# Kernel optimization log

Measured on AMD Instinct MI355X. Metric: run time of the kernel, lower is better.

Reference implementation:

```python
import jax, jax.numpy as jnp
import numpy as np
from jax import lax

B = 2048
C = 8
H = W = 14
NP = H * W  # 196
DIM = 192
THETA = 0.7


def _unfold3(z):
    # z: [B, C, H, W] -> patches [B, C, 9, H, W], matching F.unfold(kernel=3, pad=1)
    p = jnp.pad(z, ((0, 0), (0, 0), (1, 1), (1, 1)))
    return jnp.stack([p[:, :, dy:dy + H, dx:dx + W]
                      for dy in range(3) for dx in range(3)], axis=2)


def setup_inputs() -> dict:
    key = jax.random.key(0)
    ks = jax.random.split(key, 10)
    s = 0.1
    return {
        "x": jax.random.normal(ks[0], (B, 1 + NP, DIM), dtype=jnp.float32),
        "W1": jax.random.normal(ks[1], (C, DIM), dtype=jnp.float32) * s,      # linear1 192->8
        "b1": jax.random.normal(ks[2], (C,), dtype=jnp.float32) * s,
        "conv1_w": jax.random.normal(ks[3], (C, C), dtype=jnp.float32) * s,   # 1x1 conv
        "conv1_b": jax.random.normal(ks[4], (C,), dtype=jnp.float32) * s,
        "cdc_w": jax.random.normal(ks[5], (C, C, 1, 5), dtype=jnp.float32) * s,
        "wc1": jax.random.normal(ks[6], (C, C), dtype=jnp.float32) * s,       # WConv1 (1x1)
        "wc2": jax.random.normal(ks[7], (C, C), dtype=jnp.float32) * s,       # WConv2 (1x1)
        "hist_w": jax.random.normal(ks[8], (DIM, C), dtype=jnp.float32) * s,  # linear 8->192
        "hist_b": jax.random.normal(ks[9], (DIM,), dtype=jnp.float32) * s,
    }


def reference(x, W1, b1, conv1_w, conv1_b, cdc_w, wc1, wc2, hist_w, hist_b):
    class_token, tok = x[:, :1, :], x[:, 1:, :]
    # linear1: [B,196,192] -> [B,196,8]
    t = jnp.einsum('bnd,cd->bnc', tok, W1) + b1
    # -> [B,8,14,14]
    t = t.reshape(-1, H, W, C).transpose(0, 3, 1, 2)

    # conv1 (1x1)
    x1 = jnp.einsum('bihw,oi->bohw', t, conv1_w) + conv1_b[None, :, None, None]

    # CDC: scatter the 1x5 weights into a 3x3 cross-shaped kernel
    w5 = cdc_w[:, :, 0, :]  # [O,I,5]
    z = jnp.zeros((C, C, 1), dtype=cdc_w.dtype)
    k9 = jnp.concatenate([z, w5[:, :, 0:1], z,
                          w5[:, :, 1:2], w5[:, :, 2:3], w5[:, :, 3:4],
                          z, w5[:, :, 4:5], z], axis=2).reshape(C, C, 3, 3)
    out_normal = lax.conv_general_dilated(
        t, k9, window_strides=(1, 1), padding=((1, 1), (1, 1)),
        dimension_numbers=('NCHW', 'OIHW', 'NCHW'))
    kernel_diff = cdc_w.sum(axis=(2, 3))  # [O,I]
    out_diff = jnp.einsum('bihw,oi->bohw', t, kernel_diff)
    x2 = out_normal - THETA * out_diff

    z_star = x1 + x2  # [B,8,14,14]

    # TokenHistogram
    mu = jnp.einsum('bihw,oi->bohw', z_star, wc1)
    gamma = jnp.einsum('bihw,oi->bohw', z_star, wc2)
    zp = _unfold3(z_star)   # [B,8,9,14,14]
    mp = _unfold3(mu)
    gp = _unfold3(gamma)
    u = gp * (zp - mp)
    z_hist = jnp.exp(-u * u).sum(axis=2) / 9.0  # [B,8,14,14]
    # torch .reshape(-1, NP, 8): plain row-major reshape (mixes C and HW)
    z_hist = z_hist.reshape(-1, NP, C)
    y = jnp.einsum('bnc,dc->bnd', z_hist, hist_w) + hist_b  # [B,196,192]

    return jnp.concatenate([class_token, y], axis=1)
```

## Files before the change

kernel.cpp:

```cpp
#include <hip/hip_runtime.h>


#define DIMD 192
#define IMGS 37824

__launch_bounds__(256)
__global__ void k1_head(
    const float* __restrict__ x,
    const float* __restrict__ W1,
    const float* __restrict__ b1,
    const float* __restrict__ conv1_w,
    const float* __restrict__ conv1_b,
    const float* __restrict__ cdc_w,
    const float* __restrict__ wc1,
    const float* __restrict__ wc2,
    float* __restrict__ zh_ws,
    float* __restrict__ out)
{
    __shared__ float smem[4608];
    float* TS  = smem;
    float* PS  = smem + 2048;
    float* WB2 = smem + 4096;

    const int tid = threadIdx.x;
    const float* xb   = x   + (size_t)blockIdx.x * IMGS;
    float*       outb = out + (size_t)blockIdx.x * IMGS;

    {
        float4 z4 = make_float4(0.f, 0.f, 0.f, 0.f);
        float4 o4 = make_float4(1.f, 1.f, 1.f, 1.f);
        ((float4*)TS)[tid]       = z4;
        ((float4*)TS)[tid + 256] = z4;
        ((float4*)PS)[tid]       = o4;
        ((float4*)PS)[tid + 256] = o4;
    }
    if (tid < 64) {
        const float* c5 = cdc_w + tid * 5;
        float k0 = c5[0], k1 = c5[1], k2 = c5[2], k3 = c5[3], k4 = c5[4];
        float kd = k0 + k1 + k2 + k3 + k4;
        float* wp = WB2 + tid * 8;
        wp[0] = conv1_w[tid] + k2 - 0.7f * kd;
        wp[1] = k0; wp[2] = k1; wp[3] = k3; wp[4] = k4;
        wp[5] = wc1[tid];
        wp[6] = wc2[tid];
        wp[7] = 0.f;
    }
    __syncthreads();

    if (tid < 196) {
        const float4* rowp = (const float4*)(xb + DIMD + tid * DIMD);
        float acc[8];
        #pragma unroll
        for (int c = 0; c < 8; ++c) acc[c] = b1[c];
        #pragma unroll
        for (int blk = 0; blk < 6; ++blk) {
            float4 tv[8];
            #pragma unroll
            for (int u = 0; u < 8; ++u) tv[u] = rowp[blk * 8 + u];
            #pragma unroll
            for (int c = 0; c < 8; ++c) {
                const float* wrow = W1 + c * DIMD + blk * 32;
                #pragma unroll
                for (int u = 0; u < 8; ++u) {
                    acc[c] += tv[u].x * wrow[u * 4 + 0] + tv[u].y * wrow[u * 4 + 1]
                            + tv[u].z * wrow[u * 4 + 2] + tv[u].w * wrow[u * 4 + 3];
                }
            }
        }
        int h = tid / 14, w = tid - h * 14;
        float* tp = TS + (h + 1) * 16 + (w + 1);
        #pragma unroll
        for (int c = 0; c < 8; ++c) tp[c * 256] = acc[c];
    } else if (tid >= 208) {
        ((float4*)outb)[tid - 208] = ((const float4*)xb)[tid - 208];
    }
    __syncthreads();

    if (tid < 196) {
        int h = tid / 14, w = tid - h * 14;
        const float* tp = TS + (h + 1) * 16 + (w + 1);
        float zv[8];
        #pragma unroll
        for (int c = 0; c < 8; ++c) zv[c] = conv1_b[c];
        #pragma unroll
        for (int i = 0; i < 8; ++i) {
            float t0 = tp[i * 256];
            float tu = tp[i * 256 - 16];
            float td = tp[i * 256 + 16];
            float tl = tp[i * 256 - 1];
            float tr = tp[i * 256 + 1];
            #pragma unroll
            for (int c = 0; c < 8; ++c) {
                const float* wp = WB2 + (c * 8 + i) * 8;
                float4 wv = *(const float4*)wp;
                float wd = wp[4];
                zv[c] += wv.x * t0 + wv.y * tu + wv.z * tl + wv.w * tr + wd * td;
            }
        }
        float* pp = PS + (h + 1) * 16 + (w + 1);
        #pragma unroll
        for (int c = 0; c < 8; ++c) {
            float mu = 0.f, ga = 0.f;
            #pragma unroll
            for (int i = 0; i < 8; ++i) {
                const float* wp = WB2 + (c * 8 + i) * 8;
                mu += wp[5] * zv[i];
                ga += wp[6] * zv[i];
            }
            float e = ga * (zv[c] - mu);
            pp[c * 256] = __expf(-e * e);
        }
    }
    __syncthreads();

    if (tid < 196) {
        int h = tid / 14, w = tid - h * 14;
        const float* pb = PS + h * 16 + w;
        float* zg = zh_ws + (size_t)blockIdx.x * 1568;
        #pragma unroll
        for (int c = 0; c < 8; ++c) {
            const float* pr = pb + c * 256;
            float s9 = pr[0]  + pr[1]  + pr[2]
                     + pr[16] + pr[17] + pr[18]
                     + pr[32] + pr[33] + pr[34];
            zg[c * 196 + tid] = s9 * (1.f / 9.f);
        }
    }
}

__launch_bounds__(192)
__global__ void k2_hist(
    const float* __restrict__ zh_ws,
    const float* __restrict__ hist_w,
    const float* __restrict__ hist_b,
    float* __restrict__ out)
{
    __shared__ float zsh[1568];
    const int d = threadIdx.x;
    const float* zg = zh_ws + (size_t)blockIdx.x * 1568;

    for (int f = d; f < 392; f += 192)
        ((float4*)zsh)[f] = ((const float4*)zg)[f];

    const float4 h0 = *(const float4*)(hist_w + d * 8);
    const float4 h1 = *(const float4*)(hist_w + d * 8 + 4);
    const float  hb = hist_b[d];
    __syncthreads();

    float* oy = out + (size_t)blockIdx.x * IMGS + DIMD;
    #pragma unroll 4
    for (int n2 = 0; n2 < 196; ++n2) {
        const float4 z0 = *(const float4*)(zsh + n2 * 8);
        const float4 z1 = *(const float4*)(zsh + n2 * 8 + 4);
        oy[n2 * DIMD + d] = hb
            + z0.x * h0.x + z0.y * h0.y + z0.z * h0.z + z0.w * h0.w
            + z1.x * h1.x + z1.y * h1.y + z1.z * h1.z + z1.w * h1.w;
    }
}

__launch_bounds__(256)
__global__ void sadapter_fused(
    const float* __restrict__ x,
    const float* __restrict__ W1,
    const float* __restrict__ b1,
    const float* __restrict__ conv1_w,
    const float* __restrict__ conv1_b,
    const float* __restrict__ cdc_w,
    const float* __restrict__ wc1,
    const float* __restrict__ wc2,
    const float* __restrict__ hist_w,
    const float* __restrict__ hist_b,
    float* __restrict__ out)
{
    __shared__ float smem[4608];
    float* TS  = smem;
    float* ZH  = smem;
    float* PS  = smem + 2048;
    float* WB2 = smem + 4096;
    const int tid = threadIdx.x;
    const float* xb   = x   + (size_t)blockIdx.x * IMGS;
    float*       outb = out + (size_t)blockIdx.x * IMGS;

    {
        float4 z4 = make_float4(0.f,0.f,0.f,0.f), o4 = make_float4(1.f,1.f,1.f,1.f);
        ((float4*)TS)[tid] = z4; ((float4*)TS)[tid+256] = z4;
        ((float4*)PS)[tid] = o4; ((float4*)PS)[tid+256] = o4;
    }
    if (tid < 64) {
        const float* c5 = cdc_w + tid * 5;
        float k0=c5[0],k1=c5[1],k2=c5[2],k3=c5[3],k4=c5[4];
        float kd = k0+k1+k2+k3+k4;
        float* wp = WB2 + tid*8;
        wp[0]=conv1_w[tid]+k2-0.7f*kd; wp[1]=k0; wp[2]=k1; wp[3]=k3; wp[4]=k4;
        wp[5]=wc1[tid]; wp[6]=wc2[tid]; wp[7]=0.f;
    }
    __syncthreads();
    if (tid < 196) {
        const float4* rowp = (const float4*)(xb + DIMD + tid * DIMD);
        float acc[8];
        #pragma unroll
        for (int c=0;c<8;++c) acc[c]=b1[c];
        #pragma unroll
        for (int blk=0; blk<6; ++blk) {
            float4 tv[8];
            #pragma unroll
            for (int u=0;u<8;++u) tv[u]=rowp[blk*8+u];
            #pragma unroll
            for (int c=0;c<8;++c) {
                const float* wrow = W1 + c*DIMD + blk*32;
                #pragma unroll
                for (int u=0;u<8;++u)
                    acc[c] += tv[u].x*wrow[u*4+0]+tv[u].y*wrow[u*4+1]
                            + tv[u].z*wrow[u*4+2]+tv[u].w*wrow[u*4+3];
            }
        }
        int h=tid/14, w=tid-h*14;
        float* tp = TS + (h+1)*16 + (w+1);
        #pragma unroll
        for (int c=0;c<8;++c) tp[c*256]=acc[c];
    } else if (tid >= 208) {
        ((float4*)outb)[tid-208] = ((const float4*)xb)[tid-208];
    }
    __syncthreads();
    if (tid < 196) {
        int h=tid/14, w=tid-h*14;
        const float* tp = TS + (h+1)*16 + (w+1);
        float zv[8];
        #pragma unroll
        for (int c=0;c<8;++c) zv[c]=conv1_b[c];
        #pragma unroll
        for (int i=0;i<8;++i) {
            float t0=tp[i*256], tu=tp[i*256-16], td=tp[i*256+16], tl=tp[i*256-1], tr=tp[i*256+1];
            #pragma unroll
            for (int c=0;c<8;++c) {
                const float* wp = WB2 + (c*8+i)*8;
                float4 wv = *(const float4*)wp;
                zv[c] += wv.x*t0 + wv.y*tu + wv.z*tl + wv.w*tr + wp[4]*td;
            }
        }
        float* pp = PS + (h+1)*16 + (w+1);
        #pragma unroll
        for (int c=0;c<8;++c) {
            float mu=0.f, ga=0.f;
            #pragma unroll
            for (int i=0;i<8;++i) {
                const float* wp = WB2 + (c*8+i)*8;
                mu += wp[5]*zv[i]; ga += wp[6]*zv[i];
            }
            float e = ga*(zv[c]-mu);
            pp[c*256] = __expf(-e*e);
        }
    }
    __syncthreads();
    const int l  = tid & 63;
    const int wv = tid >> 6;
    const float4 ha0 = *(const float4*)(hist_w + l * 8);
    const float4 ha1 = *(const float4*)(hist_w + l * 8 + 4);
    const float4 hb0 = *(const float4*)(hist_w + (l + 64) * 8);
    const float4 hb1 = *(const float4*)(hist_w + (l + 64) * 8 + 4);
    const float4 hc0 = *(const float4*)(hist_w + (l + 128) * 8);
    const float4 hc1 = *(const float4*)(hist_w + (l + 128) * 8 + 4);
    const float  ba  = hist_b[l];
    const float  bb  = hist_b[l + 64];
    const float  bc  = hist_b[l + 128];
    if (tid < 196) {
        int h=tid/14, w=tid-h*14;
        const float* pb = PS + h*16 + w;
        #pragma unroll
        for (int c=0;c<8;++c) {
            const float* pr = pb + c*256;
            float s9 = pr[0]+pr[1]+pr[2]+pr[16]+pr[17]+pr[18]+pr[32]+pr[33]+pr[34];
            ZH[c*196+tid] = s9*(1.f/9.f);
        }
    }
    __syncthreads();
    {
        float* oy = outb + DIMD;
        const int n2beg = wv * 49;
        #pragma unroll 2
        for (int k = 0; k < 49; ++k) {
            const int n2 = n2beg + k;
            const float4 z0 = *(const float4*)(ZH + n2 * 8);
            const float4 z1 = *(const float4*)(ZH + n2 * 8 + 4);
            float a0 = ba + z0.x*ha0.x + z0.y*ha0.y + z0.z*ha0.z + z0.w*ha0.w
                          + z1.x*ha1.x + z1.y*ha1.y + z1.z*ha1.z + z1.w*ha1.w;
            float a1 = bb + z0.x*hb0.x + z0.y*hb0.y + z0.z*hb0.z + z0.w*hb0.w
                          + z1.x*hb1.x + z1.y*hb1.y + z1.z*hb1.z + z1.w*hb1.w;
            float a2 = bc + z0.x*hc0.x + z0.y*hc0.y + z0.z*hc0.z + z0.w*hc0.w
                          + z1.x*hc1.x + z1.y*hc1.y + z1.z*hc1.z + z1.w*hc1.w;
            float* orow = oy + n2 * DIMD;
            orow[l]       = a0;
            orow[l + 64]  = a1;
            orow[l + 128] = a2;
        }
    }
}

extern "C" void kernel_launch(void* const* d_in, const int* in_sizes, int n_in,
                              void* d_out, int out_size, void* d_ws, size_t ws_size,
                              hipStream_t stream)
{
    const float* x       = (const float*)d_in[0];
    const float* W1      = (const float*)d_in[1];
    const float* b1      = (const float*)d_in[2];
    const float* conv1_w = (const float*)d_in[3];
    const float* conv1_b = (const float*)d_in[4];
    const float* cdc_w   = (const float*)d_in[5];
    const float* wc1     = (const float*)d_in[6];
    const float* wc2     = (const float*)d_in[7];
    const float* hist_w  = (const float*)d_in[8];
    const float* hist_b  = (const float*)d_in[9];
    float* out = (float*)d_out;

    const size_t need = (size_t)2048 * 1568 * sizeof(float);
    if (ws_size >= need) {
        float* zh_ws = (float*)d_ws;
        k1_head<<<2048, 256, 0, stream>>>(x, W1, b1, conv1_w, conv1_b, cdc_w,
                                          wc1, wc2, zh_ws, out);
        k2_hist<<<2048, 192, 0, stream>>>(zh_ws, hist_w, hist_b, out);
    } else {
        sadapter_fused<<<2048, 256, 0, stream>>>(
            x, W1, b1, conv1_w, conv1_b, cdc_w, wc1, wc2, hist_w, hist_b, out);
    }
}
```

Before: 169.5 us.

## Merge head and histogram kernels into one launch with per-image flag handoff

Replaces the two back-to-back kernels with a single grid of interleaved producer and consumer blocks. Even blocks compute the per-image histogram features and publish them with a fence and flag, and odd blocks spin on that flag before writing the 192-wide output. The output stores also become nontemporal. The goal is to let the histogram output writes overlap with the head computation of other images and to remove the kernel boundary. The cost is a memset of the flags, spin-waiting consumer blocks that occupy CU slots, and forward progress that depends on producer blocks being scheduled before or alongside their consumers.

```diff
diff --git a/kernel.cpp b/kernel.cpp
--- a/kernel.cpp
+++ b/kernel.cpp
@@ -3,9 +3,13 @@
 
 #define DIMD 192
 #define IMGS 37824
+#define NIMG 2048
+#define ZHWORDS 1568
+
+typedef float vfloat4 __attribute__((ext_vector_type(4)));
 
 __launch_bounds__(256)
-__global__ void k1_head(
+__global__ void sadapter_ht(
     const float* __restrict__ x,
     const float* __restrict__ W1,
     const float* __restrict__ b1,
@@ -14,147 +18,179 @@
     const float* __restrict__ cdc_w,
     const float* __restrict__ wc1,
     const float* __restrict__ wc2,
+    const float* __restrict__ hist_w,
+    const float* __restrict__ hist_b,
     float* __restrict__ zh_ws,
+    int*   __restrict__ flags,
     float* __restrict__ out)
 {
     __shared__ float smem[4608];
-    float* TS  = smem;
-    float* PS  = smem + 2048;
-    float* WB2 = smem + 4096;
-
     const int tid = threadIdx.x;
-    const float* xb   = x   + (size_t)blockIdx.x * IMGS;
-    float*       outb = out + (size_t)blockIdx.x * IMGS;
-
-    {
-        float4 z4 = make_float4(0.f, 0.f, 0.f, 0.f);
-        float4 o4 = make_float4(1.f, 1.f, 1.f, 1.f);
-        ((float4*)TS)[tid]       = z4;
-        ((float4*)TS)[tid + 256] = z4;
-        ((float4*)PS)[tid]       = o4;
-        ((float4*)PS)[tid + 256] = o4;
-    }
-    if (tid < 64) {
-        const float* c5 = cdc_w + tid * 5;
-        float k0 = c5[0], k1 = c5[1], k2 = c5[2], k3 = c5[3], k4 = c5[4];
-        float kd = k0 + k1 + k2 + k3 + k4;
-        float* wp = WB2 + tid * 8;
-        wp[0] = conv1_w[tid] + k2 - 0.7f * kd;
-        wp[1] = k0; wp[2] = k1; wp[3] = k3; wp[4] = k4;
-        wp[5] = wc1[tid];
-        wp[6] = wc2[tid];
-        wp[7] = 0.f;
-    }
-    __syncthreads();
-
-    if (tid < 196) {
-        const float4* rowp = (const float4*)(xb + DIMD + tid * DIMD);
-        float acc[8];
-        #pragma unroll
-        for (int c = 0; c < 8; ++c) acc[c] = b1[c];
-        #pragma unroll
-        for (int blk = 0; blk < 6; ++blk) {
-            float4 tv[8];
-            #pragma unroll
-            for (int u = 0; u < 8; ++u) tv[u] = rowp[blk * 8 + u];
+    const int img = blockIdx.x >> 1;
+    const bool is_head = (blockIdx.x & 1) == 0;
+
+    if (is_head) {
+        float* TS  = smem;
+        float* PS  = smem + 2048;
+        float* WB2 = smem + 4096;
+        const float* xb   = x   + (size_t)img * IMGS;
+        float*       outb = out + (size_t)img * IMGS;
+
+        {
+            float4 z4 = make_float4(0.f, 0.f, 0.f, 0.f);
+            float4 o4 = make_float4(1.f, 1.f, 1.f, 1.f);
+            ((float4*)TS)[tid]       = z4;
+            ((float4*)TS)[tid + 256] = z4;
+            ((float4*)PS)[tid]       = o4;
+            ((float4*)PS)[tid + 256] = o4;
+        }
+        if (tid < 64) {
+            const float* c5 = cdc_w + tid * 5;
+            float k0 = c5[0], k1 = c5[1], k2 = c5[2], k3 = c5[3], k4 = c5[4];
+            float kd = k0 + k1 + k2 + k3 + k4;
+            float* wp = WB2 + tid * 8;
+            wp[0] = conv1_w[tid] + k2 - 0.7f * kd;
+            wp[1] = k0; wp[2] = k1; wp[3] = k3; wp[4] = k4;
+            wp[5] = wc1[tid];
+            wp[6] = wc2[tid];
+            wp[7] = 0.f;
+        }
+        __syncthreads();
+
+        if (tid < 196) {
+            const float4* rowp = (const float4*)(xb + DIMD + tid * DIMD);
+            float acc[8];
+            #pragma unroll
+            for (int c = 0; c < 8; ++c) acc[c] = b1[c];
+            #pragma unroll
+            for (int blk = 0; blk < 6; ++blk) {
+                float4 tv[8];
+                #pragma unroll
+                for (int u = 0; u < 8; ++u) tv[u] = rowp[blk * 8 + u];
+                #pragma unroll
+                for (int c = 0; c < 8; ++c) {
+                    const float* wrow = W1 + c * DIMD + blk * 32;
+                    #pragma unroll
+                    for (int u = 0; u < 8; ++u) {
+                        acc[c] += tv[u].x * wrow[u*4+0] + tv[u].y * wrow[u*4+1]
+                                + tv[u].z * wrow[u*4+2] + tv[u].w * wrow[u*4+3];
+                    }
+                }
+            }
+            int h = tid / 14, w = tid - h * 14;
+            float* tp = TS + (h + 1) * 16 + (w + 1);
+            #pragma unroll
+            for (int c = 0; c < 8; ++c) tp[c * 256] = acc[c];
+        } else if (tid >= 208) {
+            ((float4*)outb)[tid - 208] = ((const float4*)xb)[tid - 208];
+        }
+        __syncthreads();
+
+        if (tid < 196) {
+            int h = tid / 14, w = tid - h * 14;
+            const float* tp = TS + (h + 1) * 16 + (w + 1);
+            float zv[8];
+            #pragma unroll
+            for (int c = 0; c < 8; ++c) zv[c] = conv1_b[c];
+            #pragma unroll
+            for (int i = 0; i < 8; ++i) {
+                float t0 = tp[i * 256];
+                float tu = tp[i * 256 - 16];
+                float td = tp[i * 256 + 16];
+                float tl = tp[i * 256 - 1];
+                float tr = tp[i * 256 + 1];
+                #pragma unroll
+                for (int c = 0; c < 8; ++c) {
+                    const float* wp = WB2 + (c * 8 + i) * 8;
+                    float4 wv = *(const float4*)wp;
+                    float wd = wp[4];
+                    zv[c] += wv.x * t0 + wv.y * tu + wv.z * tl + wv.w * tr + wd * td;
+                }
+            }
+            float* pp = PS + (h + 1) * 16 + (w + 1);
             #pragma unroll
             for (int c = 0; c < 8; ++c) {
-                const float* wrow = W1 + c * DIMD + blk * 32;
-                #pragma unroll
-                for (int u = 0; u < 8; ++u) {
-                    acc[c] += tv[u].x * wrow[u * 4 + 0] + tv[u].y * wrow[u * 4 + 1]
-                            + tv[u].z * wrow[u * 4 + 2] + tv[u].w * wrow[u * 4 + 3];
+                float mu = 0.f, ga = 0.f;
+                #pragma unroll
+                for (int i = 0; i < 8; ++i) {
+                    const float* wp = WB2 + (c * 8 + i) * 8;
+                    mu += wp[5] * zv[i];
+                    ga += wp[6] * zv[i];
                 }
-            }
-        }
-        int h = tid / 14, w = tid - h * 14;
-        float* tp = TS + (h + 1) * 16 + (w + 1);
-        #pragma unroll
-        for (int c = 0; c < 8; ++c) tp[c * 256] = acc[c];
-    } else if (tid >= 208) {
-        ((float4*)outb)[tid - 208] = ((const float4*)xb)[tid - 208];
-    }
-    __syncthreads();
-
-    if (tid < 196) {
-        int h = tid / 14, w = tid - h * 14;
-        const float* tp = TS + (h + 1) * 16 + (w + 1);
-        float zv[8];
-        #pragma unroll
-        for (int c = 0; c < 8; ++c) zv[c] = conv1_b[c];
-        #pragma unroll
-        for (int i = 0; i < 8; ++i) {
-            float t0 = tp[i * 256];
-            float tu = tp[i * 256 - 16];
-            float td = tp[i * 256 + 16];
-            float tl = tp[i * 256 - 1];
-            float tr = tp[i * 256 + 1];
+                float e = ga * (zv[c] - mu);
+                pp[c * 256] = __expf(-e * e);
+            }
+        }
+        __syncthreads();
+
+        if (tid < 196) {
+            int h = tid / 14, w = tid - h * 14;
+            const float* pb = PS + h * 16 + w;
+            float* zg = zh_ws + (size_t)img * ZHWORDS;
             #pragma unroll
             for (int c = 0; c < 8; ++c) {
-                const float* wp = WB2 + (c * 8 + i) * 8;
-                float4 wv = *(const float4*)wp;
-                float wd = wp[4];
-                zv[c] += wv.x * t0 + wv.y * tu + wv.z * tl + wv.w * tr + wd * td;
-            }
-        }
-        float* pp = PS + (h + 1) * 16 + (w + 1);
-        #pragma unroll
-        for (int c = 0; c < 8; ++c) {
-            float mu = 0.f, ga = 0.f;
-            #pragma unroll
-            for (int i = 0; i < 8; ++i) {
-                const float* wp = WB2 + (c * 8 + i) * 8;
-                mu += wp[5] * zv[i];
-                ga += wp[6] * zv[i];
-            }
-            float e = ga * (zv[c] - mu);
-            pp[c * 256] = __expf(-e * e);
-        }
-    }
-    __syncthreads();
-
-    if (tid < 196) {
-        int h = tid / 14, w = tid - h * 14;
-        const float* pb = PS + h * 16 + w;
-        float* zg = zh_ws + (size_t)blockIdx.x * 1568;
-        #pragma unroll
-        for (int c = 0; c < 8; ++c) {
-            const float* pr = pb + c * 256;
-            float s9 = pr[0]  + pr[1]  + pr[2]
-                     + pr[16] + pr[17] + pr[18]
-                     + pr[32] + pr[33] + pr[34];
-            zg[c * 196 + tid] = s9 * (1.f / 9.f);
-        }
-    }
-}
-
-__launch_bounds__(192)
-__global__ void k2_hist(
-    const float* __restrict__ zh_ws,
-    const float* __restrict__ hist_w,
-    const float* __restrict__ hist_b,
-    float* __restrict__ out)
-{
-    __shared__ float zsh[1568];
-    const int d = threadIdx.x;
-    const float* zg = zh_ws + (size_t)blockIdx.x * 1568;
-
-    for (int f = d; f < 392; f += 192)
-        ((float4*)zsh)[f] = ((const float4*)zg)[f];
-
-    const float4 h0 = *(const float4*)(hist_w + d * 8);
-    const float4 h1 = *(const float4*)(hist_w + d * 8 + 4);
-    const float  hb = hist_b[d];
-    __syncthreads();
-
-    float* oy = out + (size_t)blockIdx.x * IMGS + DIMD;
-    #pragma unroll 4
-    for (int n2 = 0; n2 < 196; ++n2) {
-        const float4 z0 = *(const float4*)(zsh + n2 * 8);
-        const float4 z1 = *(const float4*)(zsh + n2 * 8 + 4);
-        oy[n2 * DIMD + d] = hb
-            + z0.x * h0.x + z0.y * h0.y + z0.z * h0.z + z0.w * h0.w
-            + z1.x * h1.x + z1.y * h1.y + z1.z * h1.z + z1.w * h1.w;
+                const float* pr = pb + c * 256;
+                float s9 = pr[0]  + pr[1]  + pr[2]
+                         + pr[16] + pr[17] + pr[18]
+                         + pr[32] + pr[33] + pr[34];
+                zg[c * 196 + tid] = s9 * (1.f / 9.f);
+            }
+        }
+        __syncthreads();
+
+        if (tid == 0) {
+            __threadfence();
+            atomicExch(&flags[img], 1);
+        }
+    } else {
+        float* zsh = smem;
+        const int l  = tid & 63;
+        const int wv = tid >> 6;
+        const float4 ha0 = *(const float4*)(hist_w + l * 8);
+        const float4 ha1 = *(const float4*)(hist_w + l * 8 + 4);
+        const float4 hb0 = *(const float4*)(hist_w + (l + 64) * 8);
+        const float4 hb1 = *(const float4*)(hist_w + (l + 64) * 8 + 4);
+        const float4 hc0 = *(const float4*)(hist_w + (l + 128) * 8);
+        const float4 hc1 = *(const float4*)(hist_w + (l + 128) * 8 + 4);
+        const float  ba  = hist_b[l];
+        const float  bb  = hist_b[l + 64];
+        const float  bc_ = hist_b[l + 128];
+
+        if (tid == 0) {
+            while (__hip_atomic_load(&flags[img], __ATOMIC_ACQUIRE,
+                                     __HIP_MEMORY_SCOPE_AGENT) == 0) {
+                __builtin_amdgcn_s_sleep(8);
+            }
+        }
+        __syncthreads();
+
+        const float* zg = zh_ws + (size_t)img * ZHWORDS;
+        {
+            int f = tid;
+            ((float4*)zsh)[f] = ((const float4*)zg)[f];
+            f += 256;
+            if (f < 392) ((float4*)zsh)[f] = ((const float4*)zg)[f];
+        }
+        __syncthreads();
+
+        float* oy = out + (size_t)img * IMGS + DIMD;
+        const int n2beg = wv * 49;
+        #pragma unroll 2
+        for (int k = 0; k < 49; ++k) {
+            const int n2 = n2beg + k;
+            const float4 z0 = *(const float4*)(zsh + n2 * 8);
+            const float4 z1 = *(const float4*)(zsh + n2 * 8 + 4);
+            float a0 = ba + z0.x*ha0.x + z0.y*ha0.y + z0.z*ha0.z + z0.w*ha0.w
+                          + z1.x*ha1.x + z1.y*ha1.y + z1.z*ha1.z + z1.w*ha1.w;
+            float a1 = bb + z0.x*hb0.x + z0.y*hb0.y + z0.z*hb0.z + z0.w*hb0.w
+                          + z1.x*hb1.x + z1.y*hb1.y + z1.z*hb1.z + z1.w*hb1.w;
+            float a2 = bc_+ z0.x*hc0.x + z0.y*hc0.y + z0.z*hc0.z + z0.w*hc0.w
+                          + z1.x*hc1.x + z1.y*hc1.y + z1.z*hc1.z + z1.w*hc1.w;
+            float* orow = oy + n2 * DIMD;
+            __builtin_nontemporal_store(a0, orow + l);
+            __builtin_nontemporal_store(a1, orow + l + 64);
+            __builtin_nontemporal_store(a2, orow + l + 128);
+        }
     }
 }
 
@@ -262,7 +298,7 @@
     const float4 hc1 = *(const float4*)(hist_w + (l + 128) * 8 + 4);
     const float  ba  = hist_b[l];
     const float  bb  = hist_b[l + 64];
-    const float  bc  = hist_b[l + 128];
+    const float  bc_ = hist_b[l + 128];
     if (tid < 196) {
         int h=tid/14, w=tid-h*14;
         const float* pb = PS + h*16 + w;
@@ -286,7 +322,7 @@
                           + z1.x*ha1.x + z1.y*ha1.y + z1.z*ha1.z + z1.w*ha1.w;
             float a1 = bb + z0.x*hb0.x + z0.y*hb0.y + z0.z*hb0.z + z0.w*hb0.w
                           + z1.x*hb1.x + z1.y*hb1.y + z1.z*hb1.z + z1.w*hb1.w;
-            float a2 = bc + z0.x*hc0.x + z0.y*hc0.y + z0.z*hc0.z + z0.w*hc0.w
+            float a2 = bc_+ z0.x*hc0.x + z0.y*hc0.y + z0.z*hc0.z + z0.w*hc0.w
                           + z1.x*hc1.x + z1.y*hc1.y + z1.z*hc1.z + z1.w*hc1.w;
             float* orow = oy + n2 * DIMD;
             orow[l]       = a0;
@@ -312,14 +348,17 @@
     const float* hist_b  = (const float*)d_in[9];
     float* out = (float*)d_out;
 
-    const size_t need = (size_t)2048 * 1568 * sizeof(float);
-    if (ws_size >= need) {
+    const size_t zh_bytes   = (size_t)NIMG * ZHWORDS * sizeof(float);
+    const size_t flag_bytes = (size_t)NIMG * sizeof(int);
+    if (ws_size >= zh_bytes + flag_bytes) {
         float* zh_ws = (float*)d_ws;
-        k1_head<<<2048, 256, 0, stream>>>(x, W1, b1, conv1_w, conv1_b, cdc_w,
-                                          wc1, wc2, zh_ws, out);
-        k2_hist<<<2048, 192, 0, stream>>>(zh_ws, hist_w, hist_b, out);
+        int*   flags = (int*)((char*)d_ws + zh_bytes);
+        hipMemsetAsync(flags, 0, flag_bytes, stream);
+        sadapter_ht<<<2 * NIMG, 256, 0, stream>>>(
+            x, W1, b1, conv1_w, conv1_b, cdc_w, wc1, wc2, hist_w, hist_b,
+            zh_ws, flags, out);
     } else {
-        sadapter_fused<<<2048, 256, 0, stream>>>(
+        sadapter_fused<<<NIMG, 256, 0, stream>>>(
             x, W1, b1, conv1_w, conv1_b, cdc_w, wc1, wc2, hist_w, hist_b, out);
     }
 }
```

After: 416.9 us. 2.46x slower.

## Fuse head and histogram kernels, use packed fp16 dot products for linears

Applied to the files above, without the earlier changes.

Merges the two-kernel path into one kernel that keeps the histogram result in shared memory, removing the global workspace round trip and the second launch. A tiny pre-kernel packs W1 and hist_w into fp16 pairs, and both linear layers switch to fdot2 packed-half dot products with fp32 accumulation. This reduces ALU work and weight-load traffic, at the cost of fp16 rounding of both activations and weights, which may affect accuracy tolerance.

```diff
diff --git a/kernel.cpp b/kernel.cpp
--- a/kernel.cpp
+++ b/kernel.cpp
@@ -3,22 +3,46 @@
 
 #define DIMD 192
 #define IMGS 37824
+#define NIMG 2048
+
+typedef __fp16 half2_t __attribute__((ext_vector_type(2)));
+
+__device__ __forceinline__ half2_t u2h(unsigned u) {
+    union { unsigned u; half2_t h; } cv; cv.u = u; return cv.h;
+}
+__device__ __forceinline__ unsigned h2u(half2_t h) {
+    union { half2_t h; unsigned u; } cv; cv.h = h; return cv.u;
+}
+
+__global__ void k0_pack(const float* __restrict__ W1,
+                        const float* __restrict__ hist_w,
+                        unsigned* __restrict__ wsA,
+                        unsigned* __restrict__ wsD)
+{
+    int f = threadIdx.x + blockIdx.x * 256;
+    if (f < 768) {
+        wsA[f] = h2u(__builtin_amdgcn_cvt_pkrtz(W1[2*f], W1[2*f+1]));
+        wsD[f] = h2u(__builtin_amdgcn_cvt_pkrtz(hist_w[2*f], hist_w[2*f+1]));
+    }
+}
 
 __launch_bounds__(256)
-__global__ void k1_head(
+__global__ void sadapter_kernel(
     const float* __restrict__ x,
-    const float* __restrict__ W1,
     const float* __restrict__ b1,
     const float* __restrict__ conv1_w,
     const float* __restrict__ conv1_b,
     const float* __restrict__ cdc_w,
     const float* __restrict__ wc1,
     const float* __restrict__ wc2,
-    float* __restrict__ zh_ws,
+    const unsigned* __restrict__ wsA,
+    const unsigned* __restrict__ wsD,
+    const float* __restrict__ hist_b,
     float* __restrict__ out)
 {
     __shared__ float smem[4608];
     float* TS  = smem;
+    float* ZH  = smem;
     float* PS  = smem + 2048;
     float* WB2 = smem + 4096;
 
@@ -57,14 +81,18 @@
             float4 tv[8];
             #pragma unroll
             for (int u = 0; u < 8; ++u) tv[u] = rowp[blk * 8 + u];
+            half2_t tp16[16];
+            #pragma unroll
+            for (int u = 0; u < 8; ++u) {
+                tp16[2*u]   = __builtin_amdgcn_cvt_pkrtz(tv[u].x, tv[u].y);
+                tp16[2*u+1] = __builtin_amdgcn_cvt_pkrtz(tv[u].z, tv[u].w);
+            }
             #pragma unroll
             for (int c = 0; c < 8; ++c) {
-                const float* wrow = W1 + c * DIMD + blk * 32;
+                const unsigned* wp = wsA + c * 96 + blk * 16;
                 #pragma unroll
-                for (int u = 0; u < 8; ++u) {
-                    acc[c] += tv[u].x * wrow[u * 4 + 0] + tv[u].y * wrow[u * 4 + 1]
-                            + tv[u].z * wrow[u * 4 + 2] + tv[u].w * wrow[u * 4 + 3];
-                }
+                for (int j = 0; j < 16; ++j)
+                    acc[c] = __builtin_amdgcn_fdot2(tp16[j], u2h(wp[j]), acc[c], false);
             }
         }
         int h = tid / 14, w = tid - h * 14;
@@ -113,48 +141,59 @@
     }
     __syncthreads();
 
+    const int l  = tid & 63;
+    const int wv = tid >> 6;
+    const uint4 wa = *(const uint4*)(wsD + l * 4);
+    const uint4 wb = *(const uint4*)(wsD + (l + 64) * 4);
+    const uint4 wc = *(const uint4*)(wsD + (l + 128) * 4);
+    const float ba  = hist_b[l];
+    const float bb  = hist_b[l + 64];
+    const float bc_ = hist_b[l + 128];
+
     if (tid < 196) {
         int h = tid / 14, w = tid - h * 14;
         const float* pb = PS + h * 16 + w;
-        float* zg = zh_ws + (size_t)blockIdx.x * 1568;
         #pragma unroll
         for (int c = 0; c < 8; ++c) {
             const float* pr = pb + c * 256;
             float s9 = pr[0]  + pr[1]  + pr[2]
                      + pr[16] + pr[17] + pr[18]
                      + pr[32] + pr[33] + pr[34];
-            zg[c * 196 + tid] = s9 * (1.f / 9.f);
-        }
-    }
-}
-
-__launch_bounds__(192)
-__global__ void k2_hist(
-    const float* __restrict__ zh_ws,
-    const float* __restrict__ hist_w,
-    const float* __restrict__ hist_b,
-    float* __restrict__ out)
-{
-    __shared__ float zsh[1568];
-    const int d = threadIdx.x;
-    const float* zg = zh_ws + (size_t)blockIdx.x * 1568;
-
-    for (int f = d; f < 392; f += 192)
-        ((float4*)zsh)[f] = ((const float4*)zg)[f];
-
-    const float4 h0 = *(const float4*)(hist_w + d * 8);
-    const float4 h1 = *(const float4*)(hist_w + d * 8 + 4);
-    const float  hb = hist_b[d];
-    __syncthreads();
-
-    float* oy = out + (size_t)blockIdx.x * IMGS + DIMD;
-    #pragma unroll 4
-    for (int n2 = 0; n2 < 196; ++n2) {
-        const float4 z0 = *(const float4*)(zsh + n2 * 8);
-        const float4 z1 = *(const float4*)(zsh + n2 * 8 + 4);
-        oy[n2 * DIMD + d] = hb
-            + z0.x * h0.x + z0.y * h0.y + z0.z * h0.z + z0.w * h0.w
-            + z1.x * h1.x + z1.y * h1.y + z1.z * h1.z + z1.w * h1.w;
+            ZH[c * 196 + tid] = s9 * (1.f / 9.f);
+        }
+    }
+    __syncthreads();
+
+    {
+        float* oy = outb + DIMD;
+        const int n2beg = wv * 49;
+        #pragma unroll 2
+        for (int k = 0; k < 49; ++k) {
+            const int n2 = n2beg + k;
+            const float4 z0 = *(const float4*)(ZH + n2 * 8);
+            const float4 z1 = *(const float4*)(ZH + n2 * 8 + 4);
+            half2_t zp0 = __builtin_amdgcn_cvt_pkrtz(z0.x, z0.y);
+            half2_t zp1 = __builtin_amdgcn_cvt_pkrtz(z0.z, z0.w);
+            half2_t zp2 = __builtin_amdgcn_cvt_pkrtz(z1.x, z1.y);
+            half2_t zp3 = __builtin_amdgcn_cvt_pkrtz(z1.z, z1.w);
+            float a0 = ba, a1 = bb, a2 = bc_;
+            a0 = __builtin_amdgcn_fdot2(zp0, u2h(wa.x), a0, false);
+            a0 = __builtin_amdgcn_fdot2(zp1, u2h(wa.y), a0, false);
+            a0 = __builtin_amdgcn_fdot2(zp2, u2h(wa.z), a0, false);
+            a0 = __builtin_amdgcn_fdot2(zp3, u2h(wa.w), a0, false);
+            a1 = __builtin_amdgcn_fdot2(zp0, u2h(wb.x), a1, false);
+            a1 = __builtin_amdgcn_fdot2(zp1, u2h(wb.y), a1, false);
+            a1 = __builtin_amdgcn_fdot2(zp2, u2h(wb.z), a1, false);
+            a1 = __builtin_amdgcn_fdot2(zp3, u2h(wb.w), a1, false);
+            a2 = __builtin_amdgcn_fdot2(zp0, u2h(wc.x), a2, false);
+            a2 = __builtin_amdgcn_fdot2(zp1, u2h(wc.y), a2, false);
+            a2 = __builtin_amdgcn_fdot2(zp2, u2h(wc.z), a2, false);
+            a2 = __builtin_amdgcn_fdot2(zp3, u2h(wc.w), a2, false);
+            float* orow = oy + n2 * DIMD;
+            orow[l]       = a0;
+            orow[l + 64]  = a1;
+            orow[l + 128] = a2;
+        }
     }
 }
 
@@ -262,7 +301,7 @@
     const float4 hc1 = *(const float4*)(hist_w + (l + 128) * 8 + 4);
     const float  ba  = hist_b[l];
     const float  bb  = hist_b[l + 64];
-    const float  bc  = hist_b[l + 128];
+    const float  bc_ = hist_b[l + 128];
     if (tid < 196) {
         int h=tid/14, w=tid-h*14;
         const float* pb = PS + h*16 + w;
@@ -286,7 +325,7 @@
                           + z1.x*ha1.x + z1.y*ha1.y + z1.z*ha1.z + z1.w*ha1.w;
             float a1 = bb + z0.x*hb0.x + z0.y*hb0.y + z0.z*hb0.z + z0.w*hb0.w
                           + z1.x*hb1.x + z1.y*hb1.y + z1.z*hb1.z + z1.w*hb1.w;
-            float a2 = bc + z0.x*hc0.x + z0.y*hc0.y + z0.z*hc0.z + z0.w*hc0.w
+            float a2 = bc_+ z0.x*hc0.x + z0.y*hc0.y + z0.z*hc0.z + z0.w*hc0.w
                           + z1.x*hc1.x + z1.y*hc1.y + z1.z*hc1.z + z1.w*hc1.w;
             float* orow = oy + n2 * DIMD;
             orow[l]       = a0;
@@ -312,14 +351,15 @@
     const float* hist_b  = (const float*)d_in[9];
     float* out = (float*)d_out;
 
-    const size_t need = (size_t)2048 * 1568 * sizeof(float);
+    const size_t need = 2 * 768 * sizeof(unsigned);
     if (ws_size >= need) {
-        float* zh_ws = (float*)d_ws;
-        k1_head<<<2048, 256, 0, stream>>>(x, W1, b1, conv1_w, conv1_b, cdc_w,
-                                          wc1, wc2, zh_ws, out);
-        k2_hist<<<2048, 192, 0, stream>>>(zh_ws, hist_w, hist_b, out);
+        unsigned* wsA = (unsigned*)d_ws;
+        unsigned* wsD = wsA + 768;
+        k0_pack<<<3, 256, 0, stream>>>(W1, hist_w, wsA, wsD);
+        sadapter_kernel<<<NIMG, 256, 0, stream>>>(
+            x, b1, conv1_w, conv1_b, cdc_w, wc1, wc2, wsA, wsD, hist_b, out);
     } else {
-        sadapter_fused<<<2048, 256, 0, stream>>>(
+        sadapter_fused<<<NIMG, 256, 0, stream>>>(
             x, W1, b1, conv1_w, conv1_b, cdc_w, wc1, wc2, hist_w, hist_b, out);
     }
 }
```

Measured after the change: 152.8 us. -9.9%, faster.
